# Performance work log

Hardware: AMD Instinct MI355X
Metric: run time of the kernel (lower is better)

## Reference

```python
import math
import jax, jax.numpy as jnp
from jax import lax
import numpy as np

B, C, M, N = 8, 512, 64, 64
DN = ('NCHW', 'OIHW', 'NCHW')


def dct_mat(n):
    # Orthonormal DCT-II basis, matching the torch construction.
    i = jnp.arange(n, dtype=jnp.float32)
    A = jnp.cos(jnp.outer(i, i + 0.5) * (math.pi / n)) * np.float32(math.sqrt(2.0 / n))
    return A.at[0].divide(np.float32(math.sqrt(2.0)))


def setup_inputs() -> dict:
    key = jax.random.key(0)
    ks = jax.random.split(key, 7)
    s = 0.05
    x = jax.random.normal(ks[0], (B, C, M, N), dtype=jnp.float32)
    # 4 conv branches, each: 1x1 512->128, 3x3 dil=2 128->128, 1x1 128->128
    W1 = jax.random.normal(ks[1], (4, 128, 512, 1, 1), dtype=jnp.float32) * s
    b1 = jax.random.normal(ks[2], (4, 128), dtype=jnp.float32) * s
    W2 = jax.random.normal(ks[3], (4, 128, 128, 3, 3), dtype=jnp.float32) * s
    b2 = jax.random.normal(ks[4], (4, 128), dtype=jnp.float32) * s
    W3 = jax.random.normal(ks[5], (4, 128, 128, 1, 1), dtype=jnp.float32) * s
    b3 = jax.random.normal(ks[6], (4, 128), dtype=jnp.float32) * s
    return {"x": x, "W1": W1, "b1": b1, "W2": W2, "b2": b2, "W3": W3, "b3": b3}


def dct3d_topk(x):
    b, c, m, n = x.shape
    Ac, Ar, Ak = dct_mat(n), dct_mat(m), dct_mat(c)
    # separable 3D DCT: along N, then M, then C
    t = jnp.einsum('kn,bcmn->bcmk', Ac, x)
    t = jnp.einsum('km,bcmn->bckn', Ar, t)
    D = jnp.einsum('kc,bcmn->bkmn', Ak, t)
    total = b * c * m * n
    absD = jnp.abs(D)
    s = jnp.sort(absD.reshape(-1))  # ascending; kth-largest = s[total-k]
    recons = []
    for k in (total // 4, total // 16, total // 64, total // 256):
        thr = s[total - k]
        Dm = jnp.where(absD >= thr, D, jnp.float32(0))
        y = jnp.einsum('kc,bkmn->bcmn', Ak, Dm)   # inverse along C
        y = jnp.einsum('km,bckn->bcmn', Ar, y)    # inverse along M
        y = jnp.einsum('kn,bcmk->bcmn', Ac, y)    # inverse along N
        recons.append(y)
    return jnp.stack(recons)  # [4, B, C, M, N]


def conv_branch(h, w1, c1, w2, c2, w3, c3):
    h = lax.conv_general_dilated(h, w1, (1, 1), 'VALID', dimension_numbers=DN)
    h = jax.nn.relu(h + c1[None, :, None, None])
    h = lax.conv_general_dilated(h, w2, (1, 1), ((2, 2), (2, 2)), rhs_dilation=(2, 2), dimension_numbers=DN)
    h = jax.nn.relu(h + c2[None, :, None, None])
    h = lax.conv_general_dilated(h, w3, (1, 1), 'VALID', dimension_numbers=DN)
    return jax.nn.relu(h + c3[None, :, None, None])


def reference(x, W1, b1, W2, b2, W3, b3):
    d = dct3d_topk(x)
    outs = [conv_branch(d[i], W1[i], b1[i], W2[i], b2[i], W3[i], b3[i]) for i in range(4)]
    w = jax.nn.softmax(jnp.concatenate(outs, axis=1), axis=1)
    return x * w + x
```

## Files before the change

kernel.cpp:

```cpp
#include <hip/hip_runtime.h>
#include <math.h>

#define NB   8
#define NC   512
#define SP   4096
#define TOT  16777216L
static const double PI_D = 3.14159265358979323846;

typedef short s16x8 __attribute__((ext_vector_type(8)));
typedef float f32x4 __attribute__((ext_vector_type(4)));
typedef unsigned short u16;

#define OFF_T    0L
#define OFF_CAND 0L
#define OFF_CNT  8388608L
#define OFF_P2   8392704L
#define OFF_P3   9441280L
#define OFF_H2R  9965568L
#define OFF_H3R  9969664L
#define OFF_H1P  0L
#define OFF_X2   8388608L
#define OFF_THI  16777216L
#define OFF_H1   16777216L
#define OFF_D    25165824L
#define OFF_H2   25165824L
#define OFF_AK   41943040L
#define OFF_AKH  42205184L
#define OFF_AKL  42336256L
#define OFF_ACT  42467328L
#define OFF_GBF  42468352L
#define OFF_W2A  42599424L
#define OFF_W3B  42894336L
#define OFF_HIST 42927104L
#define OFF_SEL  42937344L
#define OFF_THR  42937360L
#define OFF_ACH  42937368L
#define OFF_ACL  42939416L

__device__ inline u16 bfr(float x) {
    unsigned u = __float_as_uint(x);
    unsigned r = u + 0x7fffu + ((u >> 16) & 1u);
    return (u16)(r >> 16);
}
__device__ inline float bff(u16 h) { return __uint_as_float(((unsigned)h) << 16); }

#define MFMA(a, b, c) __builtin_amdgcn_mfma_f32_16x16x32_bf16((a), (b), (c), 0, 0, 0)

__global__ void k_ctab(float* __restrict__ ctab) {
    int m = blockIdx.x * 256 + threadIdx.x;
    if (m < 2048) ctab[m] = (float)cos(PI_D * (double)m / 1024.0);
}

__global__ void k_build_mats(const float* __restrict__ ctab,
                             u16* __restrict__ Akh, u16* __restrict__ Akl,
                             u16* __restrict__ AcT, u16* __restrict__ Ach, u16* __restrict__ Acl) {
    int idx = blockIdx.x * 256 + threadIdx.x;
    if (idx < 512 * 512) {
        int i = idx >> 9, j = idx & 511;
        float c = ctab[(i * (2 * j + 1)) & 2047];
        float f = c * (i == 0 ? 0.04419417382415922f : 0.0625f);
        u16 h = bfr(f);
        Akh[idx] = h;
        Akl[idx] = bfr(f - bff(h));
    }
    if (idx < 64 * 64) {
        int i = idx >> 6, j = idx & 63;
        float c = ctab[(8 * i * (2 * j + 1)) & 2047];
        float a = c * (i == 0 ? 0.125f : 0.17677669529663687f);
        u16 ah = bfr(a);
        Ach[idx] = ah;
        Acl[idx] = bfr(a - bff(ah));
        int n = idx >> 6, np = idx & 63;
        float w = ctab[(8 * np * (2 * n + 1)) & 2047];
        AcT[idx] = bfr(w * (np == 0 ? 0.125f : 0.17677669529663687f));
    }
}

__global__ void k_zero(unsigned* __restrict__ p, int n) {
    int i = blockIdx.x * 256 + threadIdx.x;
    if (i < n) p[i] = 0u;
}

__global__ __launch_bounds__(256, 2) void k_gmm(const float* __restrict__ W1,
                                                const u16* __restrict__ Akh, const u16* __restrict__ Akl,
                                                u16* __restrict__ G) {
    __shared__ __align__(16) short Wh[128 * 40];
    __shared__ __align__(16) short Wl[128 * 40];
    __shared__ __align__(16) short Qh[128 * 40];
    __shared__ __align__(16) short Ql[128 * 40];
    const int p0 = blockIdx.y * 128, kc0 = blockIdx.x * 128;
    const int tid = threadIdx.x;
    const int lane = tid & 63, wave = tid >> 6;
    const int fr = lane & 15, qd = lane >> 4;
    const int mq = (wave >> 1) * 64, nq = (wave & 1) * 64;
    f32x4 acc[4][4];
#pragma unroll
    for (int i = 0; i < 4; ++i)
#pragma unroll
        for (int j = 0; j < 4; ++j) acc[i][j] = (f32x4){0.f, 0.f, 0.f, 0.f};
    const float* Pg = W1 + (long)p0 * 512;
    const u16* Qgh = Akh + (long)kc0 * 512;
    const u16* Qgl = Akl + (long)kc0 * 512;
    const int r0 = tid >> 2, q40 = (tid & 3) * 8;
    float4 pa4[2], pb4[2];
    s16x8 qsh[2], qsl[2];
#pragma unroll
    for (int j = 0; j < 2; ++j) {
        int r = r0 + j * 64;
        const float* src = &Pg[(long)r * 512 + q40];
        pa4[j] = *(const float4*)src;
        pb4[j] = *(const float4*)(src + 4);
        qsh[j] = *(const s16x8*)&Qgh[(long)r * 512 + q40];
        qsl[j] = *(const s16x8*)&Qgl[(long)r * 512 + q40];
    }
    for (int ch = 0; ch < 16; ++ch) {
        __syncthreads();
#pragma unroll
        for (int j = 0; j < 2; ++j) {
            int r = r0 + j * 64;
            float f[8] = {pa4[j].x, pa4[j].y, pa4[j].z, pa4[j].w,
                          pb4[j].x, pb4[j].y, pb4[j].z, pb4[j].w};
            s16x8 vh, vl;
#pragma unroll
            for (int q = 0; q < 8; ++q) {
                u16 h = bfr(f[q]);
                vh[q] = (short)h;
                vl[q] = (short)bfr(f[q] - bff(h));
            }
            *(s16x8*)&Wh[r * 40 + q40] = vh;
            *(s16x8*)&Wl[r * 40 + q40] = vl;
            *(s16x8*)&Qh[r * 40 + q40] = qsh[j];
            *(s16x8*)&Ql[r * 40 + q40] = qsl[j];
        }
        __syncthreads();
        if (ch < 15) {
            const int kn = (ch + 1) * 32;
#pragma unroll
            for (int j = 0; j < 2; ++j) {
                int r = r0 + j * 64;
                const float* src = &Pg[(long)r * 512 + kn + q40];
                pa4[j] = *(const float4*)src;
                pb4[j] = *(const float4*)(src + 4);
                qsh[j] = *(const s16x8*)&Qgh[(long)r * 512 + kn + q40];
                qsl[j] = *(const s16x8*)&Qgl[(long)r * 512 + kn + q40];
            }
        }
        s16x8 qfh[4], qfl[4];
#pragma unroll
        for (int j = 0; j < 4; ++j) {
            qfh[j] = *(const s16x8*)&Qh[(nq + 16 * j + fr) * 40 + qd * 8];
            qfl[j] = *(const s16x8*)&Ql[(nq + 16 * j + fr) * 40 + qd * 8];
        }
#pragma unroll
        for (int i = 0; i < 4; ++i) {
            s16x8 wh = *(const s16x8*)&Wh[(mq + 16 * i + fr) * 40 + qd * 8];
            s16x8 wl = *(const s16x8*)&Wl[(mq + 16 * i + fr) * 40 + qd * 8];
#pragma unroll
            for (int j = 0; j < 4; ++j) {
                acc[i][j] = MFMA(wh, qfh[j], acc[i][j]);
                acc[i][j] = MFMA(wh, qfl[j], acc[i][j]);
                acc[i][j] = MFMA(wl, qfh[j], acc[i][j]);
            }
        }
    }
#pragma unroll
    for (int i = 0; i < 4; ++i)
#pragma unroll
        for (int j = 0; j < 4; ++j) {
            int rowb = mq + 16 * i + qd * 4;
            int col = kc0 + nq + 16 * j + fr;
#pragma unroll
            for (int r = 0; r < 4; ++r)
                G[(long)(p0 + rowb + r) * 512 + col] = bfr(acc[i][j][r]);
        }
}

__global__ void k_wprep(const float* __restrict__ W2, const float* __restrict__ W3,
                        u16* __restrict__ W2a, u16* __restrict__ W3b) {
    int idx = blockIdx.x * 256 + threadIdx.x;
    if (idx < 4 * 128 * 1152) {
        int k = idx % 1152;
        int oi = idx / 1152;
        int t = k >> 7, ci = k & 127;
        W2a[idx] = bfr(W2[((long)oi * 128 + ci) * 9 + t]);
    }
    if (idx < 65536) W3b[idx] = bfr(W3[idx]);
}

__global__ __launch_bounds__(256, 3) void k_tile_fwd(const float* __restrict__ in,
                                                     u16* __restrict__ out16,
                                                     const u16* __restrict__ Ach,
                                                     const u16* __restrict__ Acl) {
    __shared__ __align__(16) short Xb[64 * 72];
    __shared__ __align__(16) short Ah[64 * 72];
    __shared__ __align__(16) short Al[64 * 72];
    __shared__ __align__(16) short Uh[64 * 72];
    __shared__ __align__(16) short Ul[64 * 72];
    const int tid = threadIdx.x;
    const long tile = blockIdx.x;
    const float* __restrict__ src = in + tile * 4096;
    u16* __restrict__ dst = out16 + tile * 4096;
    {
        const int r = tid >> 2, q16 = (tid & 3) * 16;
        const float* s = &src[r * 64 + q16];
        float4 f0 = *(const float4*)s;
        float4 f1 = *(const float4*)(s + 4);
        float4 f2 = *(const float4*)(s + 8);
        float4 f3 = *(const float4*)(s + 12);
        s16x8 v0, v1;
        v0[0] = (short)bfr(f0.x); v0[1] = (short)bfr(f0.y);
        v0[2] = (short)bfr(f0.z); v0[3] = (short)bfr(f0.w);
        v0[4] = (short)bfr(f1.x); v0[5] = (short)bfr(f1.y);
        v0[6] = (short)bfr(f1.z); v0[7] = (short)bfr(f1.w);
        v1[0] = (short)bfr(f2.x); v1[1] = (short)bfr(f2.y);
        v1[2] = (short)bfr(f2.z); v1[3] = (short)bfr(f2.w);
        v1[4] = (short)bfr(f3.x); v1[5] = (short)bfr(f3.y);
        v1[6] = (short)bfr(f3.z); v1[7] = (short)bfr(f3.w);
        *(s16x8*)&Xb[r * 72 + q16] = v0;
        *(s16x8*)&Xb[r * 72 + q16 + 8] = v1;
        *(s16x8*)&Ah[r * 72 + q16] = *(const s16x8*)&Ach[r * 64 + q16];
        *(s16x8*)&Ah[r * 72 + q16 + 8] = *(const s16x8*)&Ach[r * 64 + q16 + 8];
        *(s16x8*)&Al[r * 72 + q16] = *(const s16x8*)&Acl[r * 64 + q16];
        *(s16x8*)&Al[r * 72 + q16 + 8] = *(const s16x8*)&Acl[r * 64 + q16 + 8];
    }
    __syncthreads();
    const int lane = tid & 63, wave = tid >> 6;
    const int fr = lane & 15, qd = lane >> 4;
    const int mq = (wave >> 1) * 32, nq = (wave & 1) * 32;
    f32x4 a1[2][2];
#pragma unroll
    for (int i = 0; i < 2; ++i)
#pragma unroll
        for (int j = 0; j < 2; ++j) a1[i][j] = (f32x4){0.f, 0.f, 0.f, 0.f};
#pragma unroll
    for (int ks = 0; ks < 2; ++ks) {
        const int k0 = ks * 32 + qd * 8;
        s16x8 xp[2];
#pragma unroll
        for (int i = 0; i < 2; ++i) xp[i] = *(const s16x8*)&Xb[(mq + 16 * i + fr) * 72 + k0];
#pragma unroll
        for (int j = 0; j < 2; ++j) {
            s16x8 qh = *(const s16x8*)&Ah[(nq + 16 * j + fr) * 72 + k0];
            s16x8 ql = *(const s16x8*)&Al[(nq + 16 * j + fr) * 72 + k0];
#pragma unroll
            for (int i = 0; i < 2; ++i) {
                a1[i][j] = MFMA(xp[i], qh, a1[i][j]);
                a1[i][j] = MFMA(xp[i], ql, a1[i][j]);
            }
        }
    }
#pragma unroll
    for (int i = 0; i < 2; ++i)
#pragma unroll
        for (int j = 0; j < 2; ++j) {
            int k1 = nq + 16 * j + fr;
            int mb = mq + 16 * i + qd * 4;
            ushort4 ph, pl;
            float v0 = a1[i][j][0], v1 = a1[i][j][1], v2 = a1[i][j][2], v3 = a1[i][j][3];
            ph.x = bfr(v0); ph.y = bfr(v1); ph.z = bfr(v2); ph.w = bfr(v3);
            pl.x = bfr(v0 - bff(ph.x)); pl.y = bfr(v1 - bff(ph.y));
            pl.z = bfr(v2 - bff(ph.z)); pl.w = bfr(v3 - bff(ph.w));
            *(ushort4*)&Uh[k1 * 72 + mb] = ph;
            *(ushort4*)&Ul[k1 * 72 + mb] = pl;
        }
    __syncthreads();
    f32x4 a2[2][2];
#pragma unroll
    for (int i = 0; i < 2; ++i)
#pragma unroll
        for (int j = 0; j < 2; ++j) a2[i][j] = (f32x4){0.f, 0.f, 0.f, 0.f};
#pragma unroll
    for (int ks = 0; ks < 2; ++ks) {
        const int k0 = ks * 32 + qd * 8;
        s16x8 uh[2], ul[2];
#pragma unroll
        for (int i = 0; i < 2; ++i) {
            uh[i] = *(const s16x8*)&Uh[(mq + 16 * i + fr) * 72 + k0];
            ul[i] = *(const s16x8*)&Ul[(mq + 16 * i + fr) * 72 + k0];
        }
#pragma unroll
        for (int j = 0; j < 2; ++j) {
            s16x8 qh = *(const s16x8*)&Ah[(nq + 16 * j + fr) * 72 + k0];
            s16x8 ql = *(const s16x8*)&Al[(nq + 16 * j + fr) * 72 + k0];
#pragma unroll
            for (int i = 0; i < 2; ++i) {
                a2[i][j] = MFMA(uh[i], qh, a2[i][j]);
                a2[i][j] = MFMA(uh[i], ql, a2[i][j]);
                a2[i][j] = MFMA(ul[i], qh, a2[i][j]);
            }
        }
    }
#pragma unroll
    for (int i = 0; i < 2; ++i)
#pragma unroll
        for (int j = 0; j < 2; ++j) {
            int k2 = nq + 16 * j + fr;
            int nb = mq + 16 * i + qd * 4;
            ushort4 pk;
            pk.x = bfr(a2[i][j][0]); pk.y = bfr(a2[i][j][1]);
            pk.z = bfr(a2[i][j][2]); pk.w = bfr(a2[i][j][3]);
            *(ushort4*)&dst[k2 * 64 + nb] = pk;
        }
}

__global__ __launch_bounds__(256) void k_tsplit(const u16* __restrict__ t16,
                                                u16* __restrict__ thi) {
    __shared__ float Ls[64][65];
    const int b = blockIdx.z, cg = blockIdx.y, pg = blockIdx.x;
    const int tid = threadIdx.x;
    const u16* src = t16 + ((long)b * 512 + cg * 64) * 4096 + pg * 64;
#pragma unroll
    for (int j = 0; j < 2; ++j) {
        int idx = tid + j * 256;
        int c = idx >> 3, p8 = (idx & 7) * 8;
        s16x8 v = *(const s16x8*)&src[(long)c * 4096 + p8];
#pragma unroll
        for (int q = 0; q < 8; ++q) Ls[c][p8 + q] = bff((u16)v[q]);
    }
    __syncthreads();
#pragma unroll
    for (int j = 0; j < 2; ++j) {
        int idx = tid + j * 256;
        int p = idx >> 3, c8 = idx & 7;
        s16x8 vh;
#pragma unroll
        for (int q = 0; q < 8; ++q) vh[q] = (short)bfr(Ls[c8 * 8 + q][p]);
        long addr = ((long)b * 4096 + pg * 64 + p) * 512 + cg * 64 + c8 * 8;
        *(s16x8*)&thi[addr] = vh;
    }
}

__global__ __launch_bounds__(256, 4) void k_cgemm(const u16* __restrict__ thi,
                                                  const u16* __restrict__ Akh, const u16* __restrict__ Akl,
                                                  float* __restrict__ D, unsigned* __restrict__ g1) {
    __shared__ __align__(16) short Ph[128 * 40];
    __shared__ __align__(16) short Qh[128 * 40];
    __shared__ __align__(16) short Ql[128 * 40];
    __shared__ unsigned hh[2048];
    const int b = blockIdx.z;
    const int p0 = blockIdx.y * 128, kc0 = blockIdx.x * 128;
    const int tid = threadIdx.x;
    const int lane = tid & 63, wave = tid >> 6;
    const int fr = lane & 15, qd = lane >> 4;
    const int mq = (wave >> 1) * 64, nq = (wave & 1) * 64;
    for (int t = tid; t < 2048; t += 256) hh[t] = 0u;
    f32x4 acc[4][4];
#pragma unroll
    for (int i = 0; i < 4; ++i)
#pragma unroll
        for (int j = 0; j < 4; ++j) acc[i][j] = (f32x4){0.f, 0.f, 0.f, 0.f};
    const u16* Pgh = thi + ((long)b * 4096 + p0) * 512;
    const u16* Qgh = Akh + (long)kc0 * 512;
    const u16* Qgl = Akl + (long)kc0 * 512;
    const int r0 = tid >> 2, q40 = (tid & 3) * 8;
    s16x8 psh[2], qsh[2], qsl[2];
#pragma unroll
    for (int j = 0; j < 2; ++j) {
        int r = r0 + j * 64;
        psh[j] = *(const s16x8*)&Pgh[(long)r * 512 + q40];
        qsh[j] = *(const s16x8*)&Qgh[(long)r * 512 + q40];
        qsl[j] = *(const s16x8*)&Qgl[(long)r * 512 + q40];
    }
    for (int ch = 0; ch < 16; ++ch) {
        __syncthreads();
#pragma unroll
        for (int j = 0; j < 2; ++j) {
            int r = r0 + j * 64;
            *(s16x8*)&Ph[r * 40 + q40] = psh[j];
            *(s16x8*)&Qh[r * 40 + q40] = qsh[j];
            *(s16x8*)&Ql[r * 40 + q40] = qsl[j];
        }
        __syncthreads();
        if (ch < 15) {
            const int kn = (ch + 1) * 32;
#pragma unroll
            for (int j = 0; j < 2; ++j) {
                int r = r0 + j * 64;
                psh[j] = *(const s16x8*)&Pgh[(long)r * 512 + kn + q40];
                qsh[j] = *(const s16x8*)&Qgh[(long)r * 512 + kn + q40];
                qsl[j] = *(const s16x8*)&Qgl[(long)r * 512 + kn + q40];
            }
        }
        s16x8 qfh[4], qfl[4];
#pragma unroll
        for (int j = 0; j < 4; ++j) {
            qfh[j] = *(const s16x8*)&Qh[(nq + 16 * j + fr) * 40 + qd * 8];
            qfl[j] = *(const s16x8*)&Ql[(nq + 16 * j + fr) * 40 + qd * 8];
        }
#pragma unroll
        for (int i = 0; i < 4; ++i) {
            s16x8 ph = *(const s16x8*)&Ph[(mq + 16 * i + fr) * 40 + qd * 8];
#pragma unroll
            for (int j = 0; j < 4; ++j) {
                acc[i][j] = MFMA(ph, qfh[j], acc[i][j]);
                acc[i][j] = MFMA(ph, qfl[j], acc[i][j]);
            }
        }
    }
#pragma unroll
    for (int i = 0; i < 4; ++i)
#pragma unroll
        for (int j = 0; j < 4; ++j) {
            int rowb = mq + 16 * i + qd * 4;
            int col = kc0 + nq + 16 * j + fr;
#pragma unroll
            for (int r = 0; r < 4; ++r) {
                float v = acc[i][j][r];
                D[((long)b * 4096 + p0 + rowb + r) * 512 + col] = v;
                unsigned bin = __float_as_uint(fabsf(v)) >> 19;
                atomicAdd(&hh[bin & 2047u], 1u << ((bin >> 11) << 4));
            }
        }
    __syncthreads();
    for (int t = tid; t < 2048; t += 256) {
        unsigned c = hh[t];
        unsigned lo = c & 0xffffu, hi = c >> 16;
        if (lo) atomicAdd(&g1[t], lo);
        if (hi) atomicAdd(&g1[t + 2048], hi);
    }
}

__global__ void k_scan1(const unsigned* __restrict__ hist, unsigned* __restrict__ sel) {
    __shared__ unsigned chunk[256];
    __shared__ unsigned above[256];
    const int t = threadIdx.x;
    unsigned s = 0;
#pragma unroll
    for (int j = 0; j < 16; ++j) s += hist[t * 16 + j];
    chunk[t] = s;
    __syncthreads();
    if (t == 0) {
        unsigned a = 0;
        for (int c = 255; c >= 0; --c) { above[c] = a; a += chunk[c]; }
    }
    __syncthreads();
    const unsigned kv[4] = {4194304u, 1048576u, 262144u, 65536u};
    unsigned run = above[t];
    for (int j = 15; j >= 0; --j) {
        unsigned bin = t * 16 + j;
        unsigned hb = hist[bin];
        unsigned Sab = run;
        run += hb;
#pragma unroll
        for (int i = 0; i < 4; ++i)
            if (run >= kv[i] && Sab < kv[i]) { sel[i] = bin; sel[4 + i] = kv[i] - Sab; }
    }
}

__global__ __launch_bounds__(256) void k_compact(const float4* __restrict__ D,
                                                 const unsigned* __restrict__ sel,
                                                 unsigned* __restrict__ cand,
                                                 unsigned* __restrict__ cnt) {
    __shared__ unsigned lctr;
    if (threadIdx.x == 0) lctr = 0u;
    __syncthreads();
    const unsigned p0 = sel[0], p1 = sel[1], p2 = sel[2], p3 = sel[3];
    const int lane = threadIdx.x & 63;
    unsigned* slice = cand + (long)blockIdx.x * 4096;
    const long n4 = TOT / 4;
    for (long idx = (long)blockIdx.x * 256 + threadIdx.x; idx < n4; idx += (long)gridDim.x * 256) {
        float4 v = D[idx];
        float f[4] = {v.x, v.y, v.z, v.w};
#pragma unroll
        for (int q = 0; q < 4; ++q) {
            unsigned u = __float_as_uint(fabsf(f[q]));
            unsigned pre = u >> 19;
            bool m = (pre == p0) | (pre == p1) | (pre == p2) | (pre == p3);
            unsigned long long mask = __ballot(m);
            if (mask) {
                int leader = __ffsll((long long)mask) - 1;
// ... 51 lines not shown
    __shared__ unsigned chunk[256];
    __shared__ unsigned above[256];
    const int t = threadIdx.x;
    for (int i = 0; i < 4; ++i) {
        const unsigned* h = hist2 + i * 1024;
        unsigned r = sel[4 + i];
        unsigned s = h[t * 4] + h[t * 4 + 1] + h[t * 4 + 2] + h[t * 4 + 3];
        chunk[t] = s;
        __syncthreads();
        if (t == 0) {
            unsigned a = 0;
            for (int c = 255; c >= 0; --c) { above[c] = a; a += chunk[c]; }
        }
        __syncthreads();
        unsigned run = above[t];
        for (int j = 3; j >= 0; --j) {
            unsigned bin = t * 4 + j;
            unsigned hb = h[bin];
            unsigned Sab = run;
            run += hb;
            if (run >= r && Sab < r) { sel[8 + i] = bin; sel[12 + i] = r - Sab; }
        }
        __syncthreads();
    }
}

__global__ __launch_bounds__(256) void k_hist3c(const unsigned* __restrict__ cand,
                                                const unsigned* __restrict__ cnt,
                                                const unsigned* __restrict__ sel,
                                                unsigned* __restrict__ partial) {
    __shared__ unsigned h[2048];
    for (int i = threadIdx.x; i < 2048; i += 256) h[i] = 0u;
    __syncthreads();
    unsigned pre2[4];
#pragma unroll
    for (int i = 0; i < 4; ++i) pre2[i] = (sel[i] << 10) | sel[8 + i];
    for (int s = 0; s < 8; ++s) {
        int slice = blockIdx.x * 8 + s;
        unsigned n = cnt[slice];
        const unsigned* L = cand + (long)slice * 4096;
        for (unsigned i = threadIdx.x; i < n; i += 256) {
            unsigned u = L[i];
            unsigned p = u >> 9, low = u & 511u;
            if (p == pre2[0]) atomicAdd(&h[low], 1u);
            else if (p == pre2[1]) atomicAdd(&h[512 + low], 1u);
            else if (p == pre2[2]) atomicAdd(&h[1024 + low], 1u);
            else if (p == pre2[3]) atomicAdd(&h[1536 + low], 1u);
        }
    }
    __syncthreads();
    unsigned* dst = partial + (long)blockIdx.x * 2048;
    for (int i = threadIdx.x; i < 2048; i += 256) dst[i] = h[i];
}

__global__ void k_scan3(const unsigned* __restrict__ hist3, const unsigned* __restrict__ sel,
                        float* __restrict__ thr) {
    __shared__ unsigned chunk[256];
    __shared__ unsigned above[256];
    const int t = threadIdx.x;
    for (int i = 0; i < 4; ++i) {
        const unsigned* h = hist3 + i * 512;
        unsigned r = sel[12 + i];
        unsigned s = h[t * 2] + h[t * 2 + 1];
        chunk[t] = s;
        __syncthreads();
        if (t == 0) {
            unsigned a = 0;
            for (int c = 255; c >= 0; --c) { above[c] = a; a += chunk[c]; }
        }
        __syncthreads();
        unsigned run = above[t];
        for (int j = 1; j >= 0; --j) {
            unsigned bin = t * 2 + j;
            unsigned hb = h[bin];
            unsigned Sab = run;
            run += hb;
            if (run >= r && Sab < r)
                thr[i] = __uint_as_float((sel[i] << 19) | (sel[8 + i] << 9) | bin);
        }
        __syncthreads();
    }
}

__global__ __launch_bounds__(256, 4) void k_conv1(const float* __restrict__ D, const u16* __restrict__ Gb,
                                                  const float* __restrict__ thrp, u16* __restrict__ h1pre) {
    __shared__ __align__(16) short Pt[128 * 40];
    __shared__ __align__(16) short Qt[128 * 40];
    const int b = blockIdx.z, br = blockIdx.y, p0 = blockIdx.x * 128;
    const int z2 = br * 8 + b;
    const float thr = thrp[br];
    const int tid = threadIdx.x;
    const int lane = tid & 63, wave = tid >> 6;
    const int fr = lane & 15, qd = lane >> 4;
    const int mq = (wave >> 1) * 64, nq = (wave & 1) * 64;
    f32x4 acc[4][4];
#pragma unroll
    for (int i = 0; i < 4; ++i)
#pragma unroll
        for (int j = 0; j < 4; ++j) acc[i][j] = (f32x4){0.f, 0.f, 0.f, 0.f};
    const float* Pg = D + ((long)b * 4096 + p0) * 512;
    const u16* Qg = Gb + (long)br * 65536;
    const int r0 = tid >> 2, q40 = (tid & 3) * 8;
    float4 da[2], db[2];
#pragma unroll
    for (int j = 0; j < 2; ++j) {
        const float* src = &Pg[(long)(r0 + j * 64) * 512 + q40];
        da[j] = *(const float4*)src;
        db[j] = *(const float4*)(src + 4);
    }
    for (int ch = 0; ch < 16; ++ch) {
        const int k0 = ch * 32;
        __syncthreads();
#pragma unroll
        for (int j = 0; j < 2; ++j) {
            int r = r0 + j * 64;
            s16x8 m;
            float f[8] = {da[j].x, da[j].y, da[j].z, da[j].w, db[j].x, db[j].y, db[j].z, db[j].w};
#pragma unroll
            for (int q = 0; q < 8; ++q) m[q] = (short)(fabsf(f[q]) >= thr ? bfr(f[q]) : (u16)0);
            *(s16x8*)&Pt[r * 40 + q40] = m;
            *(s16x8*)&Qt[r * 40 + q40] = *(const s16x8*)&Qg[(long)r * 512 + k0 + q40];
        }
        __syncthreads();
        if (ch < 15) {
            const int kn = k0 + 32;
#pragma unroll
            for (int j = 0; j < 2; ++j) {
                const float* src = &Pg[(long)(r0 + j * 64) * 512 + kn + q40];
                da[j] = *(const float4*)src;
                db[j] = *(const float4*)(src + 4);
            }
        }
        s16x8 qb[4];
#pragma unroll
        for (int j = 0; j < 4; ++j) qb[j] = *(const s16x8*)&Qt[(nq + 16 * j + fr) * 40 + qd * 8];
#pragma unroll
        for (int i = 0; i < 4; ++i) {
            s16x8 pa = *(const s16x8*)&Pt[(mq + 16 * i + fr) * 40 + qd * 8];
#pragma unroll
            for (int j = 0; j < 4; ++j) acc[i][j] = MFMA(pa, qb[j], acc[i][j]);
        }
    }
#pragma unroll
    for (int i = 0; i < 4; ++i)
#pragma unroll
        for (int j = 0; j < 4; ++j) {
            int rowb = p0 + mq + 16 * i + qd * 4;
            int o = nq + 16 * j + fr;
            ushort4 pk;
            pk.x = bfr(acc[i][j][0]); pk.y = bfr(acc[i][j][1]);
            pk.z = bfr(acc[i][j][2]); pk.w = bfr(acc[i][j][3]);
            *(ushort4*)&h1pre[((long)z2 * 128 + o) * 4096 + rowb] = pk;
        }
}

__global__ __launch_bounds__(256, 4) void k_idct1(const u16* __restrict__ h1pre, const u16* __restrict__ AcT,
                                                  u16* __restrict__ X2) {
    __shared__ __align__(16) short Pt[128 * 72];
    __shared__ __align__(16) short Qt[64 * 72];
    const int b = blockIdx.z, br = blockIdx.y, m0 = blockIdx.x * 128;
    const int z2 = br * 8 + b;
    const int tid = threadIdx.x;
    const int lane = tid & 63, wave = tid >> 6;
    const int fr = lane & 15, qd = lane >> 4;
    const int mq = wave * 32;
    const u16* Pg = h1pre + (long)z2 * 524288 + (long)m0 * 64;
    f32x4 acc[2][4];
#pragma unroll
    for (int i = 0; i < 2; ++i)
#pragma unroll
        for (int j = 0; j < 4; ++j) acc[i][j] = (f32x4){0.f, 0.f, 0.f, 0.f};
#pragma unroll
    for (int j = 0; j < 4; ++j) {
        int idx = tid + j * 256;
        int r = idx >> 3, q8 = (idx & 7) * 8;
        *(s16x8*)&Pt[r * 72 + q8] = *(const s16x8*)&Pg[(long)r * 64 + q8];
    }
#pragma unroll
    for (int j = 0; j < 2; ++j) {
        int idx = tid + j * 256;
        int r = idx >> 3, q8 = (idx & 7) * 8;
        *(s16x8*)&Qt[r * 72 + q8] = *(const s16x8*)&AcT[(long)r * 64 + q8];
    }
    __syncthreads();
#pragma unroll
    for (int ks = 0; ks < 2; ++ks) {
        s16x8 pa[2], qb[4];
#pragma unroll
        for (int i = 0; i < 2; ++i) pa[i] = *(const s16x8*)&Pt[(mq + 16 * i + fr) * 72 + ks * 32 + qd * 8];
#pragma unroll
        for (int j = 0; j < 4; ++j) qb[j] = *(const s16x8*)&Qt[(16 * j + fr) * 72 + ks * 32 + qd * 8];
#pragma unroll
        for (int i = 0; i < 2; ++i)
#pragma unroll
            for (int j = 0; j < 4; ++j) acc[i][j] = MFMA(pa[i], qb[j], acc[i][j]);
    }
#pragma unroll
    for (int i = 0; i < 2; ++i)
#pragma unroll
        for (int j = 0; j < 4; ++j) {
            int Rb = m0 + mq + 16 * i + qd * 4;
            int o = Rb >> 6, y = Rb & 63;
            int xo = 16 * j + fr;
            ushort4 pk;
            pk.x = bfr(acc[i][j][0]); pk.y = bfr(acc[i][j][1]);
            pk.z = bfr(acc[i][j][2]); pk.w = bfr(acc[i][j][3]);
            *(ushort4*)&X2[(long)z2 * 524288 + ((long)xo * 128 + o) * 64 + y] = pk;
        }
}

__global__ __launch_bounds__(256, 4) void k_idct2(const u16* __restrict__ X2, const u16* __restrict__ AcT,
                                                  const float* __restrict__ b1, u16* __restrict__ h1) {
    __shared__ __align__(16) short Pt[128 * 72];
    __shared__ __align__(16) short Qt[64 * 72];
    const int b = blockIdx.z, br = blockIdx.y, m0 = blockIdx.x * 128;
    const int z2 = br * 8 + b;
    const int tid = threadIdx.x;
    const int lane = tid & 63, wave = tid >> 6;
    const int fr = lane & 15, qd = lane >> 4;
    const int mq = wave * 32;
    const u16* Pg = X2 + (long)z2 * 524288 + (long)m0 * 64;
    f32x4 acc[2][4];
#pragma unroll
    for (int i = 0; i < 2; ++i)
#pragma unroll
        for (int j = 0; j < 4; ++j) acc[i][j] = (f32x4){0.f, 0.f, 0.f, 0.f};
#pragma unroll
    for (int j = 0; j < 4; ++j) {
        int idx = tid + j * 256;
        int r = idx >> 3, q8 = (idx & 7) * 8;
        *(s16x8*)&Pt[r * 72 + q8] = *(const s16x8*)&Pg[(long)r * 64 + q8];
    }
#pragma unroll
    for (int j = 0; j < 2; ++j) {
        int idx = tid + j * 256;
        int r = idx >> 3, q8 = (idx & 7) * 8;
        *(s16x8*)&Qt[r * 72 + q8] = *(const s16x8*)&AcT[(long)r * 64 + q8];
    }
    __syncthreads();
#pragma unroll
    for (int ks = 0; ks < 2; ++ks) {
        s16x8 pa[2], qb[4];
#pragma unroll
        for (int i = 0; i < 2; ++i) pa[i] = *(const s16x8*)&Pt[(mq + 16 * i + fr) * 72 + ks * 32 + qd * 8];
#pragma unroll
        for (int j = 0; j < 4; ++j) qb[j] = *(const s16x8*)&Qt[(16 * j + fr) * 72 + ks * 32 + qd * 8];
#pragma unroll
        for (int i = 0; i < 2; ++i)
#pragma unroll
            for (int j = 0; j < 4; ++j) acc[i][j] = MFMA(pa[i], qb[j], acc[i][j]);
    }
#pragma unroll
    for (int i = 0; i < 2; ++i)
#pragma unroll
        for (int j = 0; j < 4; ++j) {
            int Rb = m0 + mq + 16 * i + qd * 4;
            int xo = Rb >> 7, o = Rb & 127;
            int yo = 16 * j + fr;
            ushort4 pk;
            const float* bg = b1 + br * 128 + o;
            pk.x = bfr(fmaxf(acc[i][j][0] + bg[0], 0.f));
            pk.y = bfr(fmaxf(acc[i][j][1] + bg[1], 0.f));
            pk.z = bfr(fmaxf(acc[i][j][2] + bg[2], 0.f));
            pk.w = bfr(fmaxf(acc[i][j][3] + bg[3], 0.f));
            *(ushort4*)&h1[(long)z2 * 524288 + ((long)yo * 64 + xo) * 128 + o] = pk;
        }
}

__global__ __launch_bounds__(256, 4) void k_conv2(const u16* __restrict__ h1, const u16* __restrict__ W2a,
                                                  const float* __restrict__ b2, u16* __restrict__ h2) {
    __shared__ __align__(16) short Pt[128 * 40];
    __shared__ __align__(16) short Qt[128 * 40];
    const int b = blockIdx.z, br = blockIdx.y, y0 = blockIdx.x * 2;
    const int z2 = br * 8 + b;
    const int tid = threadIdx.x;
    const int lane = tid & 63, wave = tid >> 6;
    const int fr = lane & 15, qd = lane >> 4;
    const int mq = (wave >> 1) * 64, nq = (wave & 1) * 64;
    f32x4 acc[4][4];
#pragma unroll
    for (int i = 0; i < 4; ++i)
#pragma unroll
        for (int j = 0; j < 4; ++j) acc[i][j] = (f32x4){0.f, 0.f, 0.f, 0.f};
    const u16* hb = h1 + (long)z2 * 524288;
    const u16* Qg = W2a + (long)br * 147456;
    const int r0 = tid >> 2, q40 = (tid & 3) * 8;
    s16x8 preg[2];
    auto loadP = [&](int ch) {
        const int t9 = ch >> 2, ci0 = (ch & 3) * 32;
        const int ky = t9 / 3, kx = t9 - 3 * ky;
        const int dy = 2 * ky - 2, dx = 2 * kx - 2;
#pragma unroll
        for (int j = 0; j < 2; ++j) {
            int r = r0 + j * 64;
            int ry = r >> 6, xx = r & 63;
            int ysrc = y0 + ry + dy, xsrc = xx + dx;
            s16x8 v = {0, 0, 0, 0, 0, 0, 0, 0};
            if ((unsigned)ysrc < 64u && (unsigned)xsrc < 64u)
                v = *(const s16x8*)&hb[((long)ysrc * 64 + xsrc) * 128 + ci0 + q40];
            preg[j] = v;
        }
    };
    loadP(0);
    for (int ch = 0; ch < 36; ++ch) {
        __syncthreads();
#pragma unroll
        for (int j = 0; j < 2; ++j) {
            int r = r0 + j * 64;
            *(s16x8*)&Pt[r * 40 + q40] = preg[j];
            *(s16x8*)&Qt[r * 40 + q40] = *(const s16x8*)&Qg[(long)r * 1152 + ch * 32 + q40];
        }
        __syncthreads();
        if (ch < 35) loadP(ch + 1);
        s16x8 qb[4];
#pragma unroll
        for (int j = 0; j < 4; ++j) qb[j] = *(const s16x8*)&Qt[(nq + 16 * j + fr) * 40 + qd * 8];
#pragma unroll
        for (int i = 0; i < 4; ++i) {
            s16x8 pa = *(const s16x8*)&Pt[(mq + 16 * i + fr) * 40 + qd * 8];
#pragma unroll
            for (int j = 0; j < 4; ++j) acc[i][j] = MFMA(pa, qb[j], acc[i][j]);
        }
    }
#pragma unroll
    for (int i = 0; i < 4; ++i)
#pragma unroll
        for (int j = 0; j < 4; ++j) {
            int rowb = mq + 16 * i + qd * 4;
            int o = nq + 16 * j + fr;
            float bb = b2[br * 128 + o];
#pragma unroll
            for (int r = 0; r < 4; ++r) {
                float v = fmaxf(acc[i][j][r] + bb, 0.f);
                h2[(long)z2 * 524288 + ((long)y0 * 64 + rowb + r) * 128 + o] = bfr(v);
            }
        }
}

__global__ __launch_bounds__(256, 4) void k_conv3(const u16* __restrict__ h2, const u16* __restrict__ W3b,
                                                  const float* __restrict__ b3, u16* __restrict__ lgn) {
    __shared__ __align__(16) short buf[18432];
    short* Pt = buf;
    short* Qt = buf + 5120;
    const int b = blockIdx.z, br = blockIdx.y, p0 = blockIdx.x * 128;
    const int z2 = br * 8 + b;
    const int m0 = blockIdx.x * 2;
    const int tid = threadIdx.x;
    const int lane = tid & 63, wave = tid >> 6;
    const int fr = lane & 15, qd = lane >> 4;
    const int mq = (wave >> 1) * 64, nq = (wave & 1) * 64;
    f32x4 acc[4][4];
#pragma unroll
    for (int i = 0; i < 4; ++i)
#pragma unroll
        for (int j = 0; j < 4; ++j) acc[i][j] = (f32x4){0.f, 0.f, 0.f, 0.f};
    const u16* Pg = h2 + (long)z2 * 524288 + (long)p0 * 128;
    const u16* Qg = W3b + (long)br * 16384;
    for (int ch = 0; ch < 4; ++ch) {
        const int k0 = ch * 32;
        __syncthreads();
#pragma unroll
        for (int j = 0; j < 2; ++j) {
            int idx = tid + j * 256;
            int r = idx >> 2, q4 = (idx & 3) * 8;
            *(s16x8*)&Pt[r * 40 + q4] = *(const s16x8*)&Pg[(long)r * 128 + k0 + q4];
            *(s16x8*)&Qt[r * 40 + q4] = *(const s16x8*)&Qg[(long)r * 128 + k0 + q4];
        }
        __syncthreads();
        s16x8 pa[4], qb[4];
#pragma unroll
        for (int i = 0; i < 4; ++i) {
            pa[i] = *(const s16x8*)&Pt[(mq + 16 * i + fr) * 40 + qd * 8];
            qb[i] = *(const s16x8*)&Qt[(nq + 16 * i + fr) * 40 + qd * 8];
        }
#pragma unroll
        for (int i = 0; i < 4; ++i)
#pragma unroll
            for (int j = 0; j < 4; ++j) acc[i][j] = MFMA(pa[i], qb[j], acc[i][j]);
    }
    __syncthreads();
#pragma unroll
    for (int i = 0; i < 4; ++i)
#pragma unroll
        for (int j = 0; j < 4; ++j) {
            int l = mq + 16 * i + qd * 4;
            int mrow = l >> 6, nn = l & 63;
            int o = nq + 16 * j + fr;
            float bb = b3[br * 128 + o];
            ushort4 pk;
            pk.x = bfr(fmaxf(acc[i][j][0] + bb, 0.f));
            pk.y = bfr(fmaxf(acc[i][j][1] + bb, 0.f));
            pk.z = bfr(fmaxf(acc[i][j][2] + bb, 0.f));
            pk.w = bfr(fmaxf(acc[i][j][3] + bb, 0.f));
            *(ushort4*)&buf[mrow * 9216 + o * 72 + nn] = pk;
        }
    __syncthreads();
#pragma unroll
    for (int t = 0; t < 16; ++t) {
        int u = tid + t * 256;
        int mrow = u >> 11;
        int rem = u & 2047;
        int cl = rem >> 4, n4 = (rem & 15) << 2;
        ushort4 v = *(const ushort4*)&buf[mrow * 9216 + cl * 72 + n4];
        long dst = (((long)b * 64 + m0 + mrow) * 512 + br * 128 + cl) * 64 + n4;
        *(ushort4*)&lgn[dst] = v;
    }
}

__global__ __launch_bounds__(256) void k_final(const float* __restrict__ x, const u16* __restrict__ lgn,
                                               float* __restrict__ out) {
    const int b = blockIdx.y, m = blockIdx.x;
    const int tid = threadIdx.x;
    const int csub = tid >> 3, oct = tid & 7;
    const u16* L = lgn + ((long)b * 64 + m) * 512 * 64;
    __shared__ float redm[32][64];
    __shared__ float reds[32][64];
    __shared__ float Mf[64], Sf[64];
    float mx[8], sm[8];
#pragma unroll
    for (int q = 0; q < 8; ++q) { mx[q] = -1e30f; sm[q] = 0.f; }
#pragma unroll 4
    for (int k = 0; k < 16; ++k) {
        int c = csub * 16 + k;
        s16x8 v8 = *(const s16x8*)&L[c * 64 + oct * 8];
#pragma unroll
        for (int q = 0; q < 8; ++q) {
            float v = bff((u16)v8[q]);
            float mn = fmaxf(mx[q], v);
            sm[q] = sm[q] * __expf(mx[q] - mn) + __expf(v - mn);
            mx[q] = mn;
        }
    }
#pragma unroll
    for (int q = 0; q < 8; ++q) {
        redm[csub][oct * 8 + q] = mx[q];
        reds[csub][oct * 8 + q] = sm[q];
    }
    __syncthreads();
    if (tid < 64) {
        float M = -1e30f;
#pragma unroll 8
        for (int g = 0; g < 32; ++g) M = fmaxf(M, redm[g][tid]);
        float S = 0.f;
#pragma unroll 8
        for (int g = 0; g < 32; ++g) S += reds[g][tid] * __expf(redm[g][tid] - M);
        Mf[tid] = M;
        Sf[tid] = 1.0f / S;
    }
    __syncthreads();
    float Mv[8], Iv[8];
#pragma unroll
    for (int q = 0; q < 8; ++q) { Mv[q] = Mf[oct * 8 + q]; Iv[q] = Sf[oct * 8 + q]; }
    const long xb = (long)b * 512 * 4096 + m * 64 + oct * 8;
#pragma unroll 4
    for (int k = 0; k < 16; ++k) {
        int c = csub * 16 + k;
        s16x8 v8 = *(const s16x8*)&L[c * 64 + oct * 8];
        long a = xb + (long)c * 4096;
        float4 x0 = *(const float4*)&x[a];
        float4 x1 = *(const float4*)&x[a + 4];
        float xf[8] = {x0.x, x0.y, x0.z, x0.w, x1.x, x1.y, x1.z, x1.w};
        float r[8];
#pragma unroll
        for (int q = 0; q < 8; ++q) {
            float w = __expf(bff((u16)v8[q]) - Mv[q]) * Iv[q];
            r[q] = xf[q] * w + xf[q];
        }
        *(float4*)&out[a] = make_float4(r[0], r[1], r[2], r[3]);
        *(float4*)&out[a + 4] = make_float4(r[4], r[5], r[6], r[7]);
    }
}

extern "C" void kernel_launch(void* const* d_in, const int* in_sizes, int n_in,
                              void* d_out, int out_size, void* d_ws, size_t ws_size,
                              hipStream_t stream) {
    (void)in_sizes; (void)n_in; (void)out_size; (void)ws_size;
    const float* x  = (const float*)d_in[0];
    const float* W1 = (const float*)d_in[1];
    const float* b1 = (const float*)d_in[2];
    const float* W2 = (const float*)d_in[3];
    const float* b2 = (const float*)d_in[4];
    const float* W3 = (const float*)d_in[5];
    const float* b3 = (const float*)d_in[6];
    float* out = (float*)d_out;
    float* ws = (float*)d_ws;

    u16*   t16  = (u16*)(ws + OFF_T);
    unsigned* cand = (unsigned*)(ws + OFF_CAND);
    unsigned* cnt  = (unsigned*)(ws + OFF_CNT);
    unsigned* p2   = (unsigned*)(ws + OFF_P2);
    unsigned* p3   = (unsigned*)(ws + OFF_P3);
    unsigned* h2r  = (unsigned*)(ws + OFF_H2R);
    unsigned* h3r  = (unsigned*)(ws + OFF_H3R);
    u16*   h1pre= (u16*)(ws + OFF_H1P);
    u16*   lgn  = (u16*)(ws + OFF_H1P);
    u16*   X2   = (u16*)(ws + OFF_X2);
    u16*   thi  = (u16*)(ws + OFF_THI);
    u16*   h1   = (u16*)(ws + OFF_H1);
    float* D    = ws + OFF_D;
    float* ctab = ws + OFF_D;
    u16*   h2   = (u16*)(ws + OFF_H2);
    u16*   Akh  = (u16*)(ws + OFF_AKH);
    u16*   Akl  = (u16*)(ws + OFF_AKL);
    u16*   AcT  = (u16*)(ws + OFF_ACT);
    u16*   Gb   = (u16*)(ws + OFF_GBF);
    u16*   W2a  = (u16*)(ws + OFF_W2A);
    u16*   W3b  = (u16*)(ws + OFF_W3B);
    unsigned* hist1 = (unsigned*)(ws + OFF_HIST);
    unsigned* sel   = (unsigned*)(ws + OFF_SEL);
    float* thr      = ws + OFF_THR;
    u16*   Ach  = (u16*)(ws + OFF_ACH);
    u16*   Acl  = (u16*)(ws + OFF_ACL);

    k_ctab<<<8, 256, 0, stream>>>(ctab);
    k_build_mats<<<1024, 256, 0, stream>>>(ctab, Akh, Akl, AcT, Ach, Acl);
    k_zero<<<16, 256, 0, stream>>>(hist1, 4096);
    k_gmm<<<dim3(4, 4), 256, 0, stream>>>(W1, Akh, Akl, Gb);
    k_wprep<<<2304, 256, 0, stream>>>(W2, W3, W2a, W3b);

    k_tile_fwd<<<4096, 256, 0, stream>>>(x, t16, Ach, Acl);
    k_tsplit<<<dim3(64, 8, 8), 256, 0, stream>>>(t16, thi);
    k_cgemm<<<dim3(4, 32, 8), 256, 0, stream>>>(thi, Akh, Akl, D, hist1);

    k_scan1<<<1, 256, 0, stream>>>(hist1, sel);
    k_compact<<<2048, 256, 0, stream>>>((const float4*)D, sel, cand, cnt);
    k_hist2c<<<256, 256, 0, stream>>>(cand, cnt, sel, p2);
    k_red<<<16, 256, 0, stream>>>(p2, h2r, 4096, 256);
    k_scan2<<<1, 256, 0, stream>>>(h2r, sel);
    k_hist3c<<<256, 256, 0, stream>>>(cand, cnt, sel, p3);
    k_red<<<8, 256, 0, stream>>>(p3, h3r, 2048, 256);
    k_scan3<<<1, 256, 0, stream>>>(h3r, sel, thr);

    k_conv1<<<dim3(32, 4, 8), 256, 0, stream>>>(D, Gb, thr, h1pre);
    k_idct1<<<dim3(64, 4, 8), 256, 0, stream>>>(h1pre, AcT, X2);
    k_idct2<<<dim3(64, 4, 8), 256, 0, stream>>>(X2, AcT, b1, h1);
    k_conv2<<<dim3(32, 4, 8), 256, 0, stream>>>(h1, W2a, b2, h2);
    k_conv3<<<dim3(32, 4, 8), 256, 0, stream>>>(h2, W3b, b3, lgn);

    k_final<<<dim3(64, 8), 256, 0, stream>>>(x, lgn, out);
}
```

Before: 478.3 us.

## Pre-swizzle GEMM weight operands into MFMA fragment order and load from global

Weight matrices (the DCT channel basis hi/lo, the fused conv1 weights, the conv2 and conv3 weights) are rearranged in setup kernels into per-lane MFMA fragment order. The GEMM kernels then load B fragments straight from global memory with one coalesced 16-byte load per lane, instead of staging them through shared memory. This removes the LDS stores and reads and the shared-memory footprint for the B tiles, which may help occupancy. In exchange, B reads now go through L2 on every k-chunk without block-level sharing, and there is a new k_gf reordering kernel. conv2 also remaps blockIdx.x to a different row order.

After: 485.6 us. Within noise of the previous version (+1.5%).

```diff
diff --git a/kernel.cpp b/kernel.cpp
--- a/kernel.cpp
+++ b/kernel.cpp
@@ -18,13 +18,15 @@
 #define OFF_P3   9441280L
 #define OFF_H2R  9965568L
 #define OFF_H3R  9969664L
+#define OFF_GF   9971712L
 #define OFF_H1P  0L
 #define OFF_X2   8388608L
 #define OFF_THI  16777216L
 #define OFF_H1   16777216L
 #define OFF_D    25165824L
 #define OFF_H2   25165824L
-#define OFF_AK   41943040L
+#define OFF_AKFH 41943040L
+#define OFF_AKFL 42074112L
 #define OFF_AKH  42205184L
 #define OFF_AKL  42336256L
 #define OFF_ACT  42467328L
@@ -53,6 +55,7 @@
 
 __global__ void k_build_mats(const float* __restrict__ ctab,
                              u16* __restrict__ Akh, u16* __restrict__ Akl,
+                             u16* __restrict__ Akfh, u16* __restrict__ Akfl,
                              u16* __restrict__ AcT, u16* __restrict__ Ach, u16* __restrict__ Acl) {
     int idx = blockIdx.x * 256 + threadIdx.x;
     if (idx < 512 * 512) {
@@ -60,8 +63,12 @@
         float c = ctab[(i * (2 * j + 1)) & 2047];
         float f = c * (i == 0 ? 0.04419417382415922f : 0.0625f);
         u16 h = bfr(f);
+        u16 l = bfr(f - bff(h));
         Akh[idx] = h;
-        Akl[idx] = bfr(f - bff(h));
+        Akl[idx] = l;
+        long fa = ((long)(i >> 4) * 16 + (j >> 5)) * 512 + ((j >> 3) & 3) * 128 + (i & 15) * 8 + (j & 7);
+        Akfh[fa] = h;
+        Akfl[fa] = l;
     }
     if (idx < 64 * 64) {
         int i = idx >> 6, j = idx & 63;
@@ -175,16 +182,42 @@
         }
 }
 
+__global__ void k_gf(const u16* __restrict__ G, u16* __restrict__ Gf) {
+    int fidx = blockIdx.x * 256 + threadIdx.x;
+    int lane = fidx & 63;
+    int of = (fidx >> 6) & 7;
+    int ch = (fidx >> 9) & 15;
+    int br = fidx >> 13;
+    int fr = lane & 15, qd = lane >> 4;
+    s16x8 v = *(const s16x8*)&G[((long)(br * 128 + of * 16 + fr)) * 512 + ch * 32 + qd * 8];
+    *(s16x8*)&Gf[(long)fidx * 8] = v;
+}
+
 __global__ void k_wprep(const float* __restrict__ W2, const float* __restrict__ W3,
-                        u16* __restrict__ W2a, u16* __restrict__ W3b) {
+                        u16* __restrict__ W2f, u16* __restrict__ W3f) {
     int idx = blockIdx.x * 256 + threadIdx.x;
-    if (idx < 4 * 128 * 1152) {
-        int k = idx % 1152;
-        int oi = idx / 1152;
-        int t = k >> 7, ci = k & 127;
-        W2a[idx] = bfr(W2[((long)oi * 128 + ci) * 9 + t]);
-    }
-    if (idx < 65536) W3b[idx] = bfr(W3[idx]);
+    if (idx < 589824) {
+        int q = idx & 7;
+        int lane = (idx >> 3) & 63;
+        int of = (idx >> 9) & 7;
+        int rest = idx >> 12;
+        int ch = rest % 36;
+        int br = rest / 36;
+        int o = of * 16 + (lane & 15);
+        int t = ch >> 2;
+        int ci = (ch & 3) * 32 + (lane >> 4) * 8 + q;
+        W2f[idx] = bfr(W2[(((long)br * 128 + o) * 128 + ci) * 9 + t]);
+    }
+    if (idx < 65536) {
+        int q = idx & 7;
+        int lane = (idx >> 3) & 63;
+        int of = (idx >> 9) & 7;
+        int ch = (idx >> 12) & 3;
+        int br = idx >> 14;
+        int o = of * 16 + (lane & 15);
+        int k = ch * 32 + (lane >> 4) * 8 + q;
+        W3f[idx] = bfr(W3[((long)br * 128 + o) * 128 + k]);
+    }
 }
 
 __global__ __launch_bounds__(256, 3) void k_tile_fwd(const float* __restrict__ in,
@@ -331,11 +364,9 @@
 }
 
 __global__ __launch_bounds__(256, 4) void k_cgemm(const u16* __restrict__ thi,
-                                                  const u16* __restrict__ Akh, const u16* __restrict__ Akl,
+                                                  const u16* __restrict__ Akfh, const u16* __restrict__ Akfl,
                                                   float* __restrict__ D, unsigned* __restrict__ g1) {
     __shared__ __align__(16) short Ph[128 * 40];
-    __shared__ __align__(16) short Qh[128 * 40];
-    __shared__ __align__(16) short Ql[128 * 40];
     __shared__ unsigned hh[2048];
     const int b = blockIdx.z;
     const int p0 = blockIdx.y * 128, kc0 = blockIdx.x * 128;
@@ -350,42 +381,30 @@
 #pragma unroll
         for (int j = 0; j < 4; ++j) acc[i][j] = (f32x4){0.f, 0.f, 0.f, 0.f};
     const u16* Pgh = thi + ((long)b * 4096 + p0) * 512;
-    const u16* Qgh = Akh + (long)kc0 * 512;
-    const u16* Qgl = Akl + (long)kc0 * 512;
     const int r0 = tid >> 2, q40 = (tid & 3) * 8;
-    s16x8 psh[2], qsh[2], qsl[2];
-#pragma unroll
-    for (int j = 0; j < 2; ++j) {
-        int r = r0 + j * 64;
-        psh[j] = *(const s16x8*)&Pgh[(long)r * 512 + q40];
-        qsh[j] = *(const s16x8*)&Qgh[(long)r * 512 + q40];
-        qsl[j] = *(const s16x8*)&Qgl[(long)r * 512 + q40];
-    }
+    s16x8 psh[2];
+#pragma unroll
+    for (int j = 0; j < 2; ++j)
+        psh[j] = *(const s16x8*)&Pgh[(long)(r0 + j * 64) * 512 + q40];
+    const long qb0 = ((long)(kc0 >> 4) + (nq >> 4)) * 16 * 512 + (long)lane * 8;
     for (int ch = 0; ch < 16; ++ch) {
         __syncthreads();
 #pragma unroll
-        for (int j = 0; j < 2; ++j) {
-            int r = r0 + j * 64;
-            *(s16x8*)&Ph[r * 40 + q40] = psh[j];
-            *(s16x8*)&Qh[r * 40 + q40] = qsh[j];
-            *(s16x8*)&Ql[r * 40 + q40] = qsl[j];
-        }
+        for (int j = 0; j < 2; ++j)
+            *(s16x8*)&Ph[(r0 + j * 64) * 40 + q40] = psh[j];
         __syncthreads();
         if (ch < 15) {
             const int kn = (ch + 1) * 32;
 #pragma unroll
-            for (int j = 0; j < 2; ++j) {
-                int r = r0 + j * 64;
-                psh[j] = *(const s16x8*)&Pgh[(long)r * 512 + kn + q40];
-                qsh[j] = *(const s16x8*)&Qgh[(long)r * 512 + kn + q40];
-                qsl[j] = *(const s16x8*)&Qgl[(long)r * 512 + kn + q40];
-            }
-        }
+            for (int j = 0; j < 2; ++j)
+                psh[j] = *(const s16x8*)&Pgh[(long)(r0 + j * 64) * 512 + kn + q40];
+        }
+        const long qbase = qb0 + (long)ch * 512;
         s16x8 qfh[4], qfl[4];
 #pragma unroll
         for (int j = 0; j < 4; ++j) {
-            qfh[j] = *(const s16x8*)&Qh[(nq + 16 * j + fr) * 40 + qd * 8];
-            qfl[j] = *(const s16x8*)&Ql[(nq + 16 * j + fr) * 40 + qd * 8];
+            qfh[j] = *(const s16x8*)&Akfh[qbase + (long)j * 8192];
+            qfl[j] = *(const s16x8*)&Akfl[qbase + (long)j * 8192];
         }
 #pragma unroll
         for (int i = 0; i < 4; ++i) {
@@ -603,10 +622,9 @@
     }
 }
 
-__global__ __launch_bounds__(256, 4) void k_conv1(const float* __restrict__ D, const u16* __restrict__ Gb,
+__global__ __launch_bounds__(256, 4) void k_conv1(const float* __restrict__ D, const u16* __restrict__ Gf,
                                                   const float* __restrict__ thrp, u16* __restrict__ h1pre) {
     __shared__ __align__(16) short Pt[128 * 40];
-    __shared__ __align__(16) short Qt[128 * 40];
     const int b = blockIdx.z, br = blockIdx.y, p0 = blockIdx.x * 128;
     const int z2 = br * 8 + b;
     const float thr = thrp[br];
@@ -620,7 +638,6 @@
 #pragma unroll
         for (int j = 0; j < 4; ++j) acc[i][j] = (f32x4){0.f, 0.f, 0.f, 0.f};
     const float* Pg = D + ((long)b * 4096 + p0) * 512;
-    const u16* Qg = Gb + (long)br * 65536;
     const int r0 = tid >> 2, q40 = (tid & 3) * 8;
     float4 da[2], db[2];
 #pragma unroll
@@ -629,6 +646,7 @@
         da[j] = *(const float4*)src;
         db[j] = *(const float4*)(src + 4);
     }
+    const long qb0 = (((long)br * 16) * 8 + (nq >> 4)) * 512 + (long)lane * 8;
     for (int ch = 0; ch < 16; ++ch) {
         const int k0 = ch * 32;
         __syncthreads();
@@ -640,7 +658,6 @@
 #pragma unroll
             for (int q = 0; q < 8; ++q) m[q] = (short)(fabsf(f[q]) >= thr ? bfr(f[q]) : (u16)0);
             *(s16x8*)&Pt[r * 40 + q40] = m;
-            *(s16x8*)&Qt[r * 40 + q40] = *(const s16x8*)&Qg[(long)r * 512 + k0 + q40];
         }
         __syncthreads();
         if (ch < 15) {
@@ -652,9 +669,10 @@
                 db[j] = *(const float4*)(src + 4);
             }
         }
+        const long qbase = qb0 + (long)ch * 4096;
         s16x8 qb[4];
 #pragma unroll
-        for (int j = 0; j < 4; ++j) qb[j] = *(const s16x8*)&Qt[(nq + 16 * j + fr) * 40 + qd * 8];
+        for (int j = 0; j < 4; ++j) qb[j] = *(const s16x8*)&Gf[qbase + (long)j * 512];
 #pragma unroll
         for (int i = 0; i < 4; ++i) {
             s16x8 pa = *(const s16x8*)&Pt[(mq + 16 * i + fr) * 40 + qd * 8];
@@ -788,11 +806,12 @@
         }
 }
 
-__global__ __launch_bounds__(256, 4) void k_conv2(const u16* __restrict__ h1, const u16* __restrict__ W2a,
+__global__ __launch_bounds__(256, 4) void k_conv2(const u16* __restrict__ h1, const u16* __restrict__ W2f,
                                                   const float* __restrict__ b2, u16* __restrict__ h2) {
     __shared__ __align__(16) short Pt[128 * 40];
-    __shared__ __align__(16) short Qt[128 * 40];
-    const int b = blockIdx.z, br = blockIdx.y, y0 = blockIdx.x * 2;
+    const int b = blockIdx.z, br = blockIdx.y;
+    const int bx = blockIdx.x;
+    const int y0 = ((bx & 7) * 4 + (bx >> 3)) * 2;
     const int z2 = br * 8 + b;
     const int tid = threadIdx.x;
     const int lane = tid & 63, wave = tid >> 6;
@@ -804,7 +823,6 @@
 #pragma unroll
         for (int j = 0; j < 4; ++j) acc[i][j] = (f32x4){0.f, 0.f, 0.f, 0.f};
     const u16* hb = h1 + (long)z2 * 524288;
-    const u16* Qg = W2a + (long)br * 147456;
     const int r0 = tid >> 2, q40 = (tid & 3) * 8;
     s16x8 preg[2];
     auto loadP = [&](int ch) {
@@ -823,19 +841,18 @@
         }
     };
     loadP(0);
+    const long qb0 = (((long)br * 36) * 8 + (nq >> 4)) * 512 + (long)lane * 8;
     for (int ch = 0; ch < 36; ++ch) {
         __syncthreads();
 #pragma unroll
-        for (int j = 0; j < 2; ++j) {
-            int r = r0 + j * 64;
-            *(s16x8*)&Pt[r * 40 + q40] = preg[j];
-            *(s16x8*)&Qt[r * 40 + q40] = *(const s16x8*)&Qg[(long)r * 1152 + ch * 32 + q40];
-        }
+        for (int j = 0; j < 2; ++j)
+            *(s16x8*)&Pt[(r0 + j * 64) * 40 + q40] = preg[j];
         __syncthreads();
         if (ch < 35) loadP(ch + 1);
+        const long qbase = qb0 + (long)ch * 4096;
         s16x8 qb[4];
 #pragma unroll
-        for (int j = 0; j < 4; ++j) qb[j] = *(const s16x8*)&Qt[(nq + 16 * j + fr) * 40 + qd * 8];
+        for (int j = 0; j < 4; ++j) qb[j] = *(const s16x8*)&W2f[qbase + (long)j * 512];
 #pragma unroll
         for (int i = 0; i < 4; ++i) {
             s16x8 pa = *(const s16x8*)&Pt[(mq + 16 * i + fr) * 40 + qd * 8];
@@ -858,11 +875,10 @@
         }
 }
 
-__global__ __launch_bounds__(256, 4) void k_conv3(const u16* __restrict__ h2, const u16* __restrict__ W3b,
+__global__ __launch_bounds__(256, 4) void k_conv3(const u16* __restrict__ h2, const u16* __restrict__ W3f,
                                                   const float* __restrict__ b3, u16* __restrict__ lgn) {
     __shared__ __align__(16) short buf[18432];
     short* Pt = buf;
-    short* Qt = buf + 5120;
     const int b = blockIdx.z, br = blockIdx.y, p0 = blockIdx.x * 128;
     const int z2 = br * 8 + b;
     const int m0 = blockIdx.x * 2;
@@ -876,7 +892,7 @@
 #pragma unroll
         for (int j = 0; j < 4; ++j) acc[i][j] = (f32x4){0.f, 0.f, 0.f, 0.f};
     const u16* Pg = h2 + (long)z2 * 524288 + (long)p0 * 128;
-    const u16* Qg = W3b + (long)br * 16384;
+    const long qb0 = (((long)br * 4) * 8 + (nq >> 4)) * 512 + (long)lane * 8;
     for (int ch = 0; ch < 4; ++ch) {
         const int k0 = ch * 32;
         __syncthreads();
@@ -885,19 +901,18 @@
             int idx = tid + j * 256;
             int r = idx >> 2, q4 = (idx & 3) * 8;
             *(s16x8*)&Pt[r * 40 + q4] = *(const s16x8*)&Pg[(long)r * 128 + k0 + q4];
-            *(s16x8*)&Qt[r * 40 + q4] = *(const s16x8*)&Qg[(long)r * 128 + k0 + q4];
-        }
-        __syncthreads();
-        s16x8 pa[4], qb[4];
+        }
+        __syncthreads();
+        const long qbase = qb0 + (long)ch * 4096;
+        s16x8 qb[4];
+#pragma unroll
+        for (int j = 0; j < 4; ++j) qb[j] = *(const s16x8*)&W3f[qbase + (long)j * 512];
 #pragma unroll
         for (int i = 0; i < 4; ++i) {
-            pa[i] = *(const s16x8*)&Pt[(mq + 16 * i + fr) * 40 + qd * 8];
-            qb[i] = *(const s16x8*)&Qt[(nq + 16 * i + fr) * 40 + qd * 8];
-        }
-#pragma unroll
-        for (int i = 0; i < 4; ++i)
-#pragma unroll
-            for (int j = 0; j < 4; ++j) acc[i][j] = MFMA(pa[i], qb[j], acc[i][j]);
+            s16x8 pa = *(const s16x8*)&Pt[(mq + 16 * i + fr) * 40 + qd * 8];
+#pragma unroll
+            for (int j = 0; j < 4; ++j) acc[i][j] = MFMA(pa, qb[j], acc[i][j]);
+        }
     }
     __syncthreads();
 #pragma unroll
@@ -1018,6 +1033,9 @@
     u16*   X2   = (u16*)(ws + OFF_X2);
     u16*   thi  = (u16*)(ws + OFF_THI);
     u16*   h1   = (u16*)(ws + OFF_H1);
+    u16*   Akfh = (u16*)(ws + OFF_AKFH);
+    u16*   Akfl = (u16*)(ws + OFF_AKFL);
+    u16*   Gf   = (u16*)(ws + OFF_GF);
     float* D    = ws + OFF_D;
     float* ctab = ws + OFF_D;
     u16*   h2   = (u16*)(ws + OFF_H2);
@@ -1025,8 +1043,8 @@
     u16*   Akl  = (u16*)(ws + OFF_AKL);
     u16*   AcT  = (u16*)(ws + OFF_ACT);
     u16*   Gb   = (u16*)(ws + OFF_GBF);
-    u16*   W2a  = (u16*)(ws + OFF_W2A);
-    u16*   W3b  = (u16*)(ws + OFF_W3B);
+    u16*   W2f  = (u16*)(ws + OFF_W2A);
+    u16*   W3f  = (u16*)(ws + OFF_W3B);
     unsigned* hist1 = (unsigned*)(ws + OFF_HIST);
     unsigned* sel   = (unsigned*)(ws + OFF_SEL);
     float* thr      = ws + OFF_THR;
@@ -1034,14 +1052,15 @@
     u16*   Acl  = (u16*)(ws + OFF_ACL);
 
     k_ctab<<<8, 256, 0, stream>>>(ctab);
-    k_build_mats<<<1024, 256, 0, stream>>>(ctab, Akh, Akl, AcT, Ach, Acl);
+    k_build_mats<<<1024, 256, 0, stream>>>(ctab, Akh, Akl, Akfh, Akfl, AcT, Ach, Acl);
     k_zero<<<16, 256, 0, stream>>>(hist1, 4096);
     k_gmm<<<dim3(4, 4), 256, 0, stream>>>(W1, Akh, Akl, Gb);
-    k_wprep<<<2304, 256, 0, stream>>>(W2, W3, W2a, W3b);
+    k_gf<<<128, 256, 0, stream>>>(Gb, Gf);
+    k_wprep<<<2304, 256, 0, stream>>>(W2, W3, W2f, W3f);
 
     k_tile_fwd<<<4096, 256, 0, stream>>>(x, t16, Ach, Acl);
     k_tsplit<<<dim3(64, 8, 8), 256, 0, stream>>>(t16, thi);
-    k_cgemm<<<dim3(4, 32, 8), 256, 0, stream>>>(thi, Akh, Akl, D, hist1);
+    k_cgemm<<<dim3(4, 32, 8), 256, 0, stream>>>(thi, Akfh, Akfl, D, hist1);
 
     k_scan1<<<1, 256, 0, stream>>>(hist1, sel);
     k_compact<<<2048, 256, 0, stream>>>((const float4*)D, sel, cand, cnt);
@@ -1052,11 +1071,11 @@
     k_red<<<8, 256, 0, stream>>>(p3, h3r, 2048, 256);
     k_scan3<<<1, 256, 0, stream>>>(h3r, sel, thr);
 
-    k_conv1<<<dim3(32, 4, 8), 256, 0, stream>>>(D, Gb, thr, h1pre);
+    k_conv1<<<dim3(32, 4, 8), 256, 0, stream>>>(D, Gf, thr, h1pre);
     k_idct1<<<dim3(64, 4, 8), 256, 0, stream>>>(h1pre, AcT, X2);
     k_idct2<<<dim3(64, 4, 8), 256, 0, stream>>>(X2, AcT, b1, h1);
-    k_conv2<<<dim3(32, 4, 8), 256, 0, stream>>>(h1, W2a, b2, h2);
-    k_conv3<<<dim3(32, 4, 8), 256, 0, stream>>>(h2, W3b, b3, lgn);
+    k_conv2<<<dim3(32, 4, 8), 256, 0, stream>>>(h1, W2f, b2, h2);
+    k_conv3<<<dim3(32, 4, 8), 256, 0, stream>>>(h2, W3f, b3, lgn);
 
     k_final<<<dim3(64, 8), 256, 0, stream>>>(x, lgn, out);
 }
```
